# Optimization experiments

Measured on AMD Instinct MI355X. Metric: run time of the kernel, lower is better.

## Reference

```python
import jax, jax.numpy as jnp
import numpy as np

NHEAD = 16


def corrcoef(X, Y):
    # X, Y: [..., S, D]; Pearson correlation between rows of X and rows of Y
    X = X - X.mean(-1, keepdims=True)
    Y = Y - Y.mean(-1, keepdims=True)
    c = jnp.einsum('...id,...jd->...ij', X, Y)            # [..., S, S]
    d = jnp.einsum('...id,...id->...i', X, Y)             # diagonal of c
    stddev = jnp.sqrt(d)
    c = c / stddev[..., :, None]
    c = c / stddev[..., None, :]
    c = jnp.clip(c, -1.0, 1.0)
    return jnp.where(jnp.isnan(c), 0.0, c)


def setup_inputs() -> dict:
    key = jax.random.key(0)
    k1, k2, k3 = jax.random.split(key, 3)
    T, B, D = 2048, 2, 1024
    query = jax.random.normal(k1, (T, B, D), dtype=jnp.float32)
    W_qkv = jax.random.normal(k2, (3 * D, D), dtype=jnp.float32) * (1.0 / np.sqrt(D))
    b_qkv = jax.random.normal(k3, (3 * D,), dtype=jnp.float32) * 0.01
    return {"query": query, "W_qkv": W_qkv, "b_qkv": b_qkv}


def reference(query, W_qkv, b_qkv):
    T, B, D = query.shape
    hd = D // NHEAD
    qkv = query @ W_qkv.T + b_qkv                          # [T, B, 3D]
    q, k, v = jnp.split(qkv, 3, axis=-1)

    def to_bhsd(x):
        return x.reshape(T, B, NHEAD, hd).transpose(1, 2, 0, 3)  # [B, H, S, hd]

    q, k, v = to_bhsd(q), to_bhsd(k), to_bhsd(v)
    corr = corrcoef(q, k)                                   # [B, H, S, S]
    corr = jax.nn.softmax(corr, axis=-1)                    # eval: dropout_p = 0
    return corr @ v                                         # [B, H, S, hd]
```

## Files before the change

### kernel.cpp

```cpp
#include <hip/hip_runtime.h>

#define S 2048
#define D 1024
#define NH 16
#define HD 64
#define N3 3072
#define M 4096

typedef short s16x8 __attribute__((ext_vector_type(8)));
typedef _Float16 f16x8 __attribute__((ext_vector_type(8)));
typedef float f32x4 __attribute__((ext_vector_type(4)));
typedef float f32x16 __attribute__((ext_vector_type(16)));
typedef unsigned int u32;
typedef u32 u32x4 __attribute__((ext_vector_type(4)));

__device__ __forceinline__ unsigned short f2bf(float f) {
  unsigned u = __builtin_bit_cast(unsigned, f);
  u += 0x7fffu + ((u >> 16) & 1u);
  return (unsigned short)(u >> 16);
}
__device__ __forceinline__ float bf2f(unsigned short h) {
  return __builtin_bit_cast(float, (unsigned)h << 16);
}
__device__ __forceinline__ unsigned short f2h(float f) {
  _Float16 h = (_Float16)f;
  return __builtin_bit_cast(unsigned short, h);
}

__device__ __forceinline__ float wsum(float v) {
  #pragma unroll
  for (int m = 1; m < 64; m <<= 1) v += __shfl_xor(v, m, 64);
  return v;
}

__device__ __forceinline__ void gload_lds16(const unsigned short* g, unsigned short* l) {
  __builtin_amdgcn_global_load_lds(
      (const __attribute__((address_space(1))) u32*)g,
      (__attribute__((address_space(3))) u32*)l, 16, 0, 0);
}
__device__ __forceinline__ void gload_lds4(const float* g, float* l) {
  __builtin_amdgcn_global_load_lds(
      (const __attribute__((address_space(1))) u32*)g,
      (__attribute__((address_space(3))) u32*)l, 4, 0, 0);
}

__global__ __launch_bounds__(256) void split_k(const float* __restrict__ q,
                                               const float* __restrict__ w,
                                               unsigned short* __restrict__ A1,
                                               unsigned short* __restrict__ A2,
                                               unsigned short* __restrict__ W1,
                                               unsigned short* __restrict__ W2) {
  const size_t gid = (size_t)blockIdx.x * 256 + threadIdx.x;
  const size_t NA = (size_t)M * D / 4;
  float4 x;
  unsigned short* p1; unsigned short* p2; size_t qi; float scale;
  if (gid < NA) {
    qi = gid;  x = ((const float4*)q)[qi];
    p1 = A1; p2 = A2; scale = 64.f;
  } else {
    qi = gid - NA;  x = ((const float4*)w)[qi];
    p1 = W1; p2 = W2; scale = 1024.f;
  }
  float e[4] = {x.x * scale, x.y * scale, x.z * scale, x.w * scale};
  unsigned short h1[4], h2[4];
  #pragma unroll
  for (int i = 0; i < 4; ++i) {
    _Float16 a = (_Float16)e[i];
    float r = e[i] - (float)a;
    _Float16 b = (_Float16)r;
    h1[i] = __builtin_bit_cast(unsigned short, a);
    h2[i] = __builtin_bit_cast(unsigned short, b);
  }
  *(ushort4*)&p1[qi * 4] = make_ushort4(h1[0], h1[1], h1[2], h1[3]);
  *(ushort4*)&p2[qi * 4] = make_ushort4(h2[0], h2[1], h2[2], h2[3]);
}

__global__ __launch_bounds__(256) void gemm_mfma(const unsigned short* __restrict__ A1,
                                                 const unsigned short* __restrict__ A2,
                                                 const unsigned short* __restrict__ W1,
                                                 const unsigned short* __restrict__ W2,
                                                 const float* __restrict__ bias,
                                                 float* __restrict__ C) {
  __shared__ unsigned short As[128 * 64];
  __shared__ unsigned short Bs[128 * 64];
  const int tid = threadIdx.x;
  const int w = tid >> 6, l = tid & 63;
  const int lo = l & 15, hi = l >> 4;
  const int n0 = blockIdx.x * 128, m0 = blockIdx.y * 128;
  const int wr = w >> 1, wc = w & 1;

  const int nseg = (n0 >= 2048) ? 1 : 3;

  const int srow = (tid >> 3) & 31;
  const int skc = tid & 7;

  f32x4 acc[4][4];
  #pragma unroll
  for (int mi = 0; mi < 4; ++mi)
    #pragma unroll
    for (int nj = 0; nj < 4; ++nj) acc[mi][nj] = (f32x4){0.f, 0.f, 0.f, 0.f};

  for (int s = 0; s < 3; ++s) {
    if (s >= nseg) break;
    const unsigned short* Ab;
    const unsigned short* Bb;
    switch (s) {
      case 0: Ab = A1; Bb = W1; break;
      case 1: Ab = A2; Bb = W1; break;
      default: Ab = A1; Bb = W2; break;
    }
    Ab += (size_t)m0 * D;
    Bb += (size_t)n0 * D;

    for (int k0 = 0; k0 < D; k0 += 64) {
      __syncthreads();
      #pragma unroll
      for (int c = 0; c < 4; ++c) {
        const int row = c * 32 + srow;
        const int koct = skc ^ (row & 7);
        gload_lds16(Ab + (size_t)row * D + k0 + koct * 8,
                    As + c * 2048 + w * 512);
        gload_lds16(Bb + (size_t)row * D + k0 + koct * 8,
                    Bs + c * 2048 + w * 512);
      }
      __syncthreads();

      f16x8 af[4][2], bf[4][2];
      #pragma unroll
      for (int mi = 0; mi < 4; ++mi)
        #pragma unroll
        for (int ks = 0; ks < 2; ++ks) {
          const int row = wr * 64 + mi * 16 + lo;
          const int koct = (ks * 4 + hi) ^ (lo & 7);
          af[mi][ks] = *(const f16x8*)&As[row * 64 + koct * 8];
        }
      #pragma unroll
      for (int nj = 0; nj < 4; ++nj)
        #pragma unroll
        for (int ks = 0; ks < 2; ++ks) {
          const int row = wc * 64 + nj * 16 + lo;
          const int koct = (ks * 4 + hi) ^ (lo & 7);
          bf[nj][ks] = *(const f16x8*)&Bs[row * 64 + koct * 8];
        }
      #pragma unroll
      for (int mi = 0; mi < 4; ++mi)
        #pragma unroll
        for (int nj = 0; nj < 4; ++nj)
          #pragma unroll
          for (int ks = 0; ks < 2; ++ks)
            acc[mi][nj] = __builtin_amdgcn_mfma_f32_16x16x32_f16(
                af[mi][ks], bf[nj][ks], acc[mi][nj], 0, 0, 0);
    }
  }

  #pragma unroll
  for (int mi = 0; mi < 4; ++mi)
    #pragma unroll
    for (int nj = 0; nj < 4; ++nj) {
      const int n = n0 + wc * 64 + nj * 16 + lo;
      const float bj = bias[n];
      #pragma unroll
      for (int r = 0; r < 4; ++r) {
        const int m = m0 + wr * 64 + mi * 16 + hi * 4 + r;
        C[(size_t)m * N3 + n] = acc[mi][nj][r] * (1.f / 65536.f) + bj;
      }
    }
}

__global__ __launch_bounds__(256) void stats_k(const float* __restrict__ qkv,
                                               unsigned short* __restrict__ qhi,
                                               unsigned short* __restrict__ qlo,
                                               unsigned short* __restrict__ khi,
                                               unsigned short* __restrict__ klo,
                                               unsigned short* __restrict__ vt,
                                               float* __restrict__ rs) {
  __shared__ unsigned short VsT[64][65];
  const int tt = blockIdx.x, bh = blockIdx.y;
  const int b = bh >> 4, h = bh & 15;
  const int w = threadIdx.x >> 6, l = threadIdx.x & 63;

  for (int rr = 0; rr < 16; ++rr) {
    const int t = tt * 64 + w * 16 + rr;
    const size_t base = (size_t)(t * 2 + b) * N3 + h * HD;
    const float q = qkv[base + l];
    const float k = qkv[base + D + l];
    const float v = qkv[base + 2 * D + l];
    const float qm = wsum(q) * (1.f / 64.f);
    const float km = wsum(k) * (1.f / 64.f);
    const float qcv = q - qm, kcv = k - km;
    const float d = wsum(qcv * kcv);
    float rv = 0.f;
    if (d > 0.f) {
      rv = rsqrtf(d);
      rv = rv * (1.5f - 0.5f * d * rv * rv);
    }
    const size_t ro = ((size_t)bh * S + t) * HD + l;
    const unsigned short qh = f2bf(qcv);
    const unsigned short kh = f2bf(kcv);
    qhi[ro] = qh;  qlo[ro] = f2bf(qcv - bf2f(qh));
    khi[ro] = kh;  klo[ro] = f2bf(kcv - bf2f(kh));
    if (l == 0) rs[(size_t)bh * S + t] = rv;
    VsT[l][w * 16 + rr] = f2h(v);
  }
  __syncthreads();
  const int dd = threadIdx.x >> 2, seg = threadIdx.x & 3;
  unsigned pk[8];
  #pragma unroll
  for (int e = 0; e < 8; ++e) {
    unsigned l2 = VsT[dd][seg * 16 + 2 * e];
    unsigned h2 = VsT[dd][seg * 16 + 2 * e + 1];
    pk[e] = l2 | (h2 << 16);
  }
  unsigned short* dst = vt + ((size_t)bh * HD + dd) * S + tt * 64 + seg * 16;
  *(uint4*)dst       = make_uint4(pk[0], pk[1], pk[2], pk[3]);
  *(uint4*)(dst + 8) = make_uint4(pk[4], pk[5], pk[6], pk[7]);
}

__global__ __launch_bounds__(256) void attn_k(const unsigned short* __restrict__ qhi,
                                              const unsigned short* __restrict__ qlo,
                                              const unsigned short* __restrict__ khi,
                                              const unsigned short* __restrict__ klo,
                                              const unsigned short* __restrict__ vt,
                                              const float* __restrict__ rs,
                                              float* __restrict__ out) {
  __shared__ unsigned short Kh[64 * 64];
  __shared__ unsigned short Kl[64 * 64];
  __shared__ unsigned short Vsm[64 * 64];
  __shared__ float Rsl[64];

  const int tid = threadIdx.x;
  const int w = tid >> 6, l = tid & 63;
  const int lq = l & 31;
  const int h = l >> 5;
  const int l7 = l & 7;

  const int wgid = blockIdx.x;
  const int orig = (wgid & 7) * 64 + (wgid >> 3);
  const int bh = orig >> 4, qt = orig & 15;

  const unsigned short* qhb = qhi + (size_t)bh * S * HD;
  const unsigned short* qlb = qlo + (size_t)bh * S * HD;
  const unsigned short* khb = khi + (size_t)bh * S * HD;
  const unsigned short* klb = klo + (size_t)bh * S * HD;
  const unsigned short* vbase = vt + (size_t)bh * HD * S;
  const float* rbase = rs + (size_t)bh * S;
  const int qrow0 = qt * 128 + w * 32;

  const int srow3 = l >> 3;
  const int sg = l7 ^ srow3;

  s16x8 qfh[4], qfl[4];
  #pragma unroll
  for (int kc = 0; kc < 4; ++kc) {
    const size_t off = (size_t)(qrow0 + lq) * HD + kc * 16 + h * 8;
    qfh[kc] = *(const s16x8*)(qhb + off);
    qfl[kc] = *(const s16x8*)(qlb + off);
  }
  const float rsq = rbase[qrow0 + lq];

  f32x16 oacc[2];
  oacc[0] = (f32x16)(0.f);
  oacc[1] = (f32x16)(0.f);
  float den = 0.f;

  for (int j0 = 0; j0 < S; j0 += 64) {
    __syncthreads();
    #pragma unroll
    for (int c = 0; c < 2; ++c) {
      const int row = c * 32 + w * 8 + srow3;
      const int dst = c * 2048 + w * 512;
      gload_lds16(khb + (size_t)(j0 + row) * HD + sg * 8, Kh + dst);
      gload_lds16(klb + (size_t)(j0 + row) * HD + sg * 8, Kl + dst);
      gload_lds16(vbase + (size_t)row * S + j0 + sg * 8, Vsm + dst);
    }
    if (w == 0) gload_lds4(rbase + j0 + l, Rsl);
    __syncthreads();

    #pragma unroll
    for (int jblk = 0; jblk < 2; ++jblk) {
      f32x16 sacc = (f32x16)(0.f);
      #pragma unroll
      for (int kc = 0; kc < 4; ++kc) {
        const int off = (jblk * 32 + lq) * 64 + (((kc * 2 + h) ^ l7) << 3);
        s16x8 akh = *(const s16x8*)&Kh[off];
        s16x8 akl = *(const s16x8*)&Kl[off];
        sacc = __builtin_amdgcn_mfma_f32_32x32x16_bf16(akh, qfh[kc], sacc, 0, 0, 0);
        sacc = __builtin_amdgcn_mfma_f32_32x32x16_bf16(akl, qfh[kc], sacc, 0, 0, 0);
        sacc = __builtin_amdgcn_mfma_f32_32x32x16_bf16(akh, qfl[kc], sacc, 0, 0, 0);
      }

      u32 pkA[4], pkB[4];
      #pragma unroll
      for (int g = 0; g < 4; ++g) {
        f32x4 rjv = *(const f32x4*)&Rsl[jblk * 32 + g * 8 + h * 4];
        float e0, e1, e2, e3;
        {
          float c0 = fminf(1.f, fmaxf(-1.f, sacc[4 * g + 0] * rsq * rjv[0]));
          float c1 = fminf(1.f, fmaxf(-1.f, sacc[4 * g + 1] * rsq * rjv[1]));
          float c2 = fminf(1.f, fmaxf(-1.f, sacc[4 * g + 2] * rsq * rjv[2]));
          float c3 = fminf(1.f, fmaxf(-1.f, sacc[4 * g + 3] * rsq * rjv[3]));
          e0 = __expf(c0); e1 = __expf(c1); e2 = __expf(c2); e3 = __expf(c3);
        }
        den += (e0 + e1) + (e2 + e3);
        pkA[g] = __builtin_bit_cast(u32, __builtin_amdgcn_cvt_pkrtz(e0, e1));
        pkB[g] = __builtin_bit_cast(u32, __builtin_amdgcn_cvt_pkrtz(e2, e3));
      }

      #pragma unroll
      for (int jc2 = 0; jc2 < 2; ++jc2) {
        const u32 sA = h ? pkA[2 * jc2] : pkA[2 * jc2 + 1];
        const u32 sB = h ? pkB[2 * jc2] : pkB[2 * jc2 + 1];
        const u32 rA = (u32)__shfl_xor((int)sA, 32, 64);
        const u32 rB = (u32)__shfl_xor((int)sB, 32, 64);
        u32x4 uu;
        uu[0] = h ? rA : pkA[2 * jc2];
        uu[1] = h ? rB : pkB[2 * jc2];
        uu[2] = h ? pkA[2 * jc2 + 1] : rA;
        uu[3] = h ? pkB[2 * jc2 + 1] : rB;
        const f16x8 pa = __builtin_bit_cast(f16x8, uu);

        const int jcg = jblk * 2 + jc2;
        #pragma unroll
        for (int dblk = 0; dblk < 2; ++dblk) {
          const int voff = (dblk * 32 + lq) * 64 + (((jcg * 2 + h) ^ l7) << 3);
          f16x8 bv = *(const f16x8*)&Vsm[voff];
          oacc[dblk] = __builtin_amdgcn_mfma_f32_32x32x16_f16(pa, bv, oacc[dblk], 0, 0, 0);
        }
      }
    }
  }

  const float dtot = den + __shfl_xor(den, 32, 64);
  const float inv = 1.f / dtot;

  #pragma unroll
  for (int g = 0; g < 4; ++g)
    #pragma unroll
    for (int i = 0; i < 4; ++i) {
      const int qr = i + 8 * g + 4 * h;
      const float invq = __shfl(inv, i + 8 * g + 4 * h, 64);
      const size_t row = (size_t)bh * S + qrow0 + qr;
      out[row * HD + lq]      = oacc[0][4 * g + i] * invq;
      out[row * HD + 32 + lq] = oacc[1][4 * g + i] * invq;
    }
}

extern "C" void kernel_launch(void* const* d_in, const int* in_sizes, int n_in,
                              void* d_out, int out_size, void* d_ws, size_t ws_size,
                              hipStream_t stream) {
  const float* query = (const float*)d_in[0];
  const float* W     = (const float*)d_in[1];
  const float* bias  = (const float*)d_in[2];
  float* out = (float*)d_out;
  char* ws = (char*)d_ws;

  float*          qkv = (float*)ws;
  unsigned short* A1 = (unsigned short*)(ws + 50331648);
  unsigned short* A2 = (unsigned short*)(ws + 58720256);
  unsigned short* W1 = (unsigned short*)(ws + 67108864);
  unsigned short* W2 = (unsigned short*)(ws + 73400320);
  unsigned short* qhi = (unsigned short*)(ws + 50331648);
  unsigned short* qlo = (unsigned short*)(ws + 58720256);
  unsigned short* khi = (unsigned short*)(ws + 67108864);
  unsigned short* klo = (unsigned short*)(ws + 75497472);
  unsigned short* vt  = (unsigned short*)(ws + 83886080);
  float*          rsb = (float*)(ws + 92274688);

  split_k  <<<dim3(7168), 256, 0, stream>>>(query, W, A1, A2, W1, W2);
  gemm_mfma<<<dim3(24, 32), 256, 0, stream>>>(A1, A2, W1, W2, bias, qkv);
  stats_k  <<<dim3(32, 32), 256, 0, stream>>>(qkv, qhi, qlo, khi, klo, vt, rsb);
  attn_k   <<<dim3(512), 256, 0, stream>>>(qhi, qlo, khi, klo, vt, rsb, out);
}
```

Baseline: 184.5 us.

## Double-buffer K/V LDS tiles and fold log2e into row scales for exp2

Splits the LDS tiles into two buffers so the next K/V/scale tile is staged while the current one is computed, leaving one barrier per iteration instead of two. Also pre-multiplies each row's inverse stddev by sqrt(log2 e) so softmax can call exp2 directly, with the clip bounds scaled to match. Doubling LDS usage may reduce occupancy, and any overlap depends on the async loads not being waited on immediately.

```diff
diff --git a/kernel.cpp b/kernel.cpp
--- a/kernel.cpp
+++ b/kernel.cpp
@@ -13,6 +13,8 @@
 typedef float f32x16 __attribute__((ext_vector_type(16)));
 typedef unsigned int u32;
 typedef u32 u32x4 __attribute__((ext_vector_type(4)));
+
+#define LOG2E 1.44269504088896340736f
 
 __device__ __forceinline__ unsigned short f2bf(float f) {
   unsigned u = __builtin_bit_cast(unsigned, f);
@@ -193,6 +195,7 @@
     if (d > 0.f) {
       rv = rsqrtf(d);
       rv = rv * (1.5f - 0.5f * d * rv * rv);
+      rv *= 1.20112240872f;
     }
     const size_t ro = ((size_t)bh * S + t) * HD + l;
     const unsigned short qh = f2bf(qcv);
@@ -223,10 +226,10 @@
                                               const unsigned short* __restrict__ vt,
                                               const float* __restrict__ rs,
                                               float* __restrict__ out) {
-  __shared__ unsigned short Kh[64 * 64];
-  __shared__ unsigned short Kl[64 * 64];
-  __shared__ unsigned short Vsm[64 * 64];
-  __shared__ float Rsl[64];
+  __shared__ unsigned short Kh[2 * 4096];
+  __shared__ unsigned short Kl[2 * 4096];
+  __shared__ unsigned short Vsm[2 * 4096];
+  __shared__ float Rsl[2 * 64];
 
   const int tid = threadIdx.x;
   const int w = tid >> 6, l = tid & 63;
@@ -263,25 +266,32 @@
   oacc[1] = (f32x16)(0.f);
   float den = 0.f;
 
-  for (int j0 = 0; j0 < S; j0 += 64) {
-    __syncthreads();
+  auto STAGE = [&](int buf, int j0) {
     #pragma unroll
     for (int c = 0; c < 2; ++c) {
       const int row = c * 32 + w * 8 + srow3;
-      const int dst = c * 2048 + w * 512;
+      const int dst = buf * 4096 + c * 2048 + w * 512;
       gload_lds16(khb + (size_t)(j0 + row) * HD + sg * 8, Kh + dst);
       gload_lds16(klb + (size_t)(j0 + row) * HD + sg * 8, Kl + dst);
       gload_lds16(vbase + (size_t)row * S + j0 + sg * 8, Vsm + dst);
     }
-    if (w == 0) gload_lds4(rbase + j0 + l, Rsl);
-    __syncthreads();
-
+    if (w == 0) gload_lds4(rbase + j0 + l, Rsl + buf * 64);
+  };
+
+  STAGE(0, 0);
+  __syncthreads();
+
+  int cur = 0;
+  for (int t = 0; t < 32; ++t) {
+    if (t < 31) STAGE(cur ^ 1, (t + 1) * 64);
+
+    const int cb = cur * 4096;
     #pragma unroll
     for (int jblk = 0; jblk < 2; ++jblk) {
       f32x16 sacc = (f32x16)(0.f);
       #pragma unroll
       for (int kc = 0; kc < 4; ++kc) {
-        const int off = (jblk * 32 + lq) * 64 + (((kc * 2 + h) ^ l7) << 3);
+        const int off = cb + (jblk * 32 + lq) * 64 + (((kc * 2 + h) ^ l7) << 3);
         s16x8 akh = *(const s16x8*)&Kh[off];
         s16x8 akl = *(const s16x8*)&Kl[off];
         sacc = __builtin_amdgcn_mfma_f32_32x32x16_bf16(akh, qfh[kc], sacc, 0, 0, 0);
@@ -292,14 +302,14 @@
       u32 pkA[4], pkB[4];
       #pragma unroll
       for (int g = 0; g < 4; ++g) {
-        f32x4 rjv = *(const f32x4*)&Rsl[jblk * 32 + g * 8 + h * 4];
+        f32x4 rjv = *(const f32x4*)&Rsl[cur * 64 + jblk * 32 + g * 8 + h * 4];
         float e0, e1, e2, e3;
         {
-          float c0 = fminf(1.f, fmaxf(-1.f, sacc[4 * g + 0] * rsq * rjv[0]));
-          float c1 = fminf(1.f, fmaxf(-1.f, sacc[4 * g + 1] * rsq * rjv[1]));
-          float c2 = fminf(1.f, fmaxf(-1.f, sacc[4 * g + 2] * rsq * rjv[2]));
-          float c3 = fminf(1.f, fmaxf(-1.f, sacc[4 * g + 3] * rsq * rjv[3]));
-          e0 = __expf(c0); e1 = __expf(c1); e2 = __expf(c2); e3 = __expf(c3);
+          float t0 = fminf(LOG2E, fmaxf(-LOG2E, sacc[4 * g + 0] * rsq * rjv[0]));
+          float t1 = fminf(LOG2E, fmaxf(-LOG2E, sacc[4 * g + 1] * rsq * rjv[1]));
+          float t2 = fminf(LOG2E, fmaxf(-LOG2E, sacc[4 * g + 2] * rsq * rjv[2]));
+          float t3 = fminf(LOG2E, fmaxf(-LOG2E, sacc[4 * g + 3] * rsq * rjv[3]));
+          e0 = exp2f(t0); e1 = exp2f(t1); e2 = exp2f(t2); e3 = exp2f(t3);
         }
         den += (e0 + e1) + (e2 + e3);
         pkA[g] = __builtin_bit_cast(u32, __builtin_amdgcn_cvt_pkrtz(e0, e1));
@@ -322,12 +332,15 @@
         const int jcg = jblk * 2 + jc2;
         #pragma unroll
         for (int dblk = 0; dblk < 2; ++dblk) {
-          const int voff = (dblk * 32 + lq) * 64 + (((jcg * 2 + h) ^ l7) << 3);
+          const int voff = cb + (dblk * 32 + lq) * 64 + (((jcg * 2 + h) ^ l7) << 3);
           f16x8 bv = *(const f16x8*)&Vsm[voff];
           oacc[dblk] = __builtin_amdgcn_mfma_f32_32x32x16_f16(pa, bv, oacc[dblk], 0, 0, 0);
         }
       }
     }
+
+    __syncthreads();
+    cur ^= 1;
   }
 
   const float dtot = den + __shfl_xor(den, 32, 64);
```

Result: slower. 193.0 us (+4.6%).

## Drop LDS staging in attention kernel, load K/V fragments directly from global

Applied to the files above, without the earlier changes.

Removes the shared-memory tiles for K hi/lo, V and row scales, along with the two barriers per key tile. Each wave now reads its MFMA operands straight from global memory, relying on the caches for reuse across the four waves in a block. This cuts synchronization and LDS traffic. In exchange it makes four times more global/L2 requests per block and issues narrow strided loads, notably 16-byte reads of V with a stride of S per row.

```diff
diff --git a/kernel.cpp b/kernel.cpp
--- a/kernel.cpp
+++ b/kernel.cpp
@@ -37,11 +37,6 @@
   __builtin_amdgcn_global_load_lds(
       (const __attribute__((address_space(1))) u32*)g,
       (__attribute__((address_space(3))) u32*)l, 16, 0, 0);
-}
-__device__ __forceinline__ void gload_lds4(const float* g, float* l) {
-  __builtin_amdgcn_global_load_lds(
-      (const __attribute__((address_space(1))) u32*)g,
-      (__attribute__((address_space(3))) u32*)l, 4, 0, 0);
 }
 
 __global__ __launch_bounds__(256) void split_k(const float* __restrict__ q,
@@ -223,17 +218,10 @@
                                               const unsigned short* __restrict__ vt,
                                               const float* __restrict__ rs,
                                               float* __restrict__ out) {
-  __shared__ unsigned short Kh[64 * 64];
-  __shared__ unsigned short Kl[64 * 64];
-  __shared__ unsigned short Vsm[64 * 64];
-  __shared__ float Rsl[64];
-
   const int tid = threadIdx.x;
   const int w = tid >> 6, l = tid & 63;
   const int lq = l & 31;
   const int h = l >> 5;
-  const int l7 = l & 7;
-
   const int wgid = blockIdx.x;
   const int orig = (wgid & 7) * 64 + (wgid >> 3);
   const int bh = orig >> 4, qt = orig & 15;
@@ -246,9 +234,6 @@
   const float* rbase = rs + (size_t)bh * S;
   const int qrow0 = qt * 128 + w * 32;
 
-  const int srow3 = l >> 3;
-  const int sg = l7 ^ srow3;
-
   s16x8 qfh[4], qfl[4];
   #pragma unroll
   for (int kc = 0; kc < 4; ++kc) {
@@ -258,32 +243,27 @@
   }
   const float rsq = rbase[qrow0 + lq];
 
+  const unsigned short* kh_l = khb + (size_t)lq * HD;
+  const unsigned short* kl_l = klb + (size_t)lq * HD;
+  const unsigned short* v_l0 = vbase + (size_t)lq * S + h * 8;
+  const unsigned short* v_l1 = vbase + (size_t)(32 + lq) * S + h * 8;
+  const int kdo = h * 8;
+
   f32x16 oacc[2];
   oacc[0] = (f32x16)(0.f);
   oacc[1] = (f32x16)(0.f);
   float den = 0.f;
 
-  for (int j0 = 0; j0 < S; j0 += 64) {
-    __syncthreads();
-    #pragma unroll
-    for (int c = 0; c < 2; ++c) {
-      const int row = c * 32 + w * 8 + srow3;
-      const int dst = c * 2048 + w * 512;
-      gload_lds16(khb + (size_t)(j0 + row) * HD + sg * 8, Kh + dst);
-      gload_lds16(klb + (size_t)(j0 + row) * HD + sg * 8, Kl + dst);
-      gload_lds16(vbase + (size_t)row * S + j0 + sg * 8, Vsm + dst);
-    }
-    if (w == 0) gload_lds4(rbase + j0 + l, Rsl);
-    __syncthreads();
-
+  for (int t = 0; t < 32; ++t) {
+    const int j0 = t * 64;
     #pragma unroll
     for (int jblk = 0; jblk < 2; ++jblk) {
+      const size_t jb = (size_t)(j0 + jblk * 32) * HD;
       f32x16 sacc = (f32x16)(0.f);
       #pragma unroll
       for (int kc = 0; kc < 4; ++kc) {
-        const int off = (jblk * 32 + lq) * 64 + (((kc * 2 + h) ^ l7) << 3);
-        s16x8 akh = *(const s16x8*)&Kh[off];
-        s16x8 akl = *(const s16x8*)&Kl[off];
+        s16x8 akh = *(const s16x8*)(kh_l + jb + kc * 16 + kdo);
+        s16x8 akl = *(const s16x8*)(kl_l + jb + kc * 16 + kdo);
         sacc = __builtin_amdgcn_mfma_f32_32x32x16_bf16(akh, qfh[kc], sacc, 0, 0, 0);
         sacc = __builtin_amdgcn_mfma_f32_32x32x16_bf16(akl, qfh[kc], sacc, 0, 0, 0);
         sacc = __builtin_amdgcn_mfma_f32_32x32x16_bf16(akh, qfl[kc], sacc, 0, 0, 0);
@@ -292,7 +272,7 @@
       u32 pkA[4], pkB[4];
       #pragma unroll
       for (int g = 0; g < 4; ++g) {
-        f32x4 rjv = *(const f32x4*)&Rsl[jblk * 32 + g * 8 + h * 4];
+        f32x4 rjv = *(const f32x4*)(rbase + j0 + jblk * 32 + g * 8 + h * 4);
         float e0, e1, e2, e3;
         {
           float c0 = fminf(1.f, fmaxf(-1.f, sacc[4 * g + 0] * rsq * rjv[0]));
@@ -319,13 +299,11 @@
         uu[3] = h ? pkB[2 * jc2 + 1] : rB;
         const f16x8 pa = __builtin_bit_cast(f16x8, uu);
 
-        const int jcg = jblk * 2 + jc2;
-        #pragma unroll
-        for (int dblk = 0; dblk < 2; ++dblk) {
-          const int voff = (dblk * 32 + lq) * 64 + (((jcg * 2 + h) ^ l7) << 3);
-          f16x8 bv = *(const f16x8*)&Vsm[voff];
-          oacc[dblk] = __builtin_amdgcn_mfma_f32_32x32x16_f16(pa, bv, oacc[dblk], 0, 0, 0);
-        }
+        const int jg = j0 + (jblk * 2 + jc2) * 16;
+        f16x8 bv0 = *(const f16x8*)(v_l0 + jg);
+        f16x8 bv1 = *(const f16x8*)(v_l1 + jg);
+        oacc[0] = __builtin_amdgcn_mfma_f32_32x32x16_f16(pa, bv0, oacc[0], 0, 0, 0);
+        oacc[1] = __builtin_amdgcn_mfma_f32_32x32x16_f16(pa, bv1, oacc[1], 0, 0, 0);
       }
     }
   }
```

Result: slower. 298.3 us (+61.7%).
